# Optimization experiments

Measured on AMD Instinct MI355X. Metric: run time of the kernel, lower is better.

The kernel has to match this reference:

```python
import jax, jax.numpy as jnp
import numpy as np

DIM = 128
HEADS = 4
WIN = (2, 7, 7)
N = WIN[0] * WIN[1] * WIN[2]  # 98
NW = 64
B_ = 2048  # batch(32) * nW(64)
SCALE = (DIM // HEADS) ** -0.5


def _relative_position_index():
    d, h, w = WIN
    coords = np.stack(np.meshgrid(np.arange(d), np.arange(h), np.arange(w), indexing='ij'))
    cf = coords.reshape(3, -1)
    rel = (cf[:, :, None] - cf[:, None, :]).transpose(1, 2, 0)
    rel[:, :, 0] += d - 1
    rel[:, :, 1] += h - 1
    rel[:, :, 2] += w - 1
    rel[:, :, 0] *= (2 * h - 1) * (2 * w - 1)
    rel[:, :, 1] *= 2 * w - 1
    return rel.sum(-1).astype(np.int32)  # [N, N]


def setup_inputs() -> dict:
    key = jax.random.key(0)
    ks = jax.random.split(key, 8)
    table_rows = (2 * WIN[0] - 1) * (2 * WIN[1] - 1) * (2 * WIN[2] - 1)  # 507
    return {
        "x": jax.random.normal(ks[0], (B_, N, DIM), jnp.float32),
        "mask": jax.random.normal(ks[1], (NW, N, N), jnp.float32),
        "qkv_w": jax.random.normal(ks[2], (DIM, 3 * DIM), jnp.float32) * 0.02,
        "qkv_b": jnp.zeros((3 * DIM,), jnp.float32),
        "rel_bias_table": jax.random.normal(ks[3], (table_rows, HEADS), jnp.float32) * 0.02,
        "rel_index": jnp.asarray(_relative_position_index()),
        "proj_w": jax.random.normal(ks[4], (DIM, DIM), jnp.float32) * 0.02,
        "proj_b": jnp.zeros((DIM,), jnp.float32),
    }


def reference(x, mask, qkv_w, qkv_b, rel_bias_table, rel_index, proj_w, proj_b):
    B, n, C = x.shape
    H = HEADS
    hd = C // H
    qkv = x @ qkv_w + qkv_b                              # [B, N, 3C]
    qkv = qkv.reshape(B, n, 3, H, hd).transpose(2, 0, 3, 1, 4)  # [3, B, H, N, hd]
    q, k, v = qkv[0] * SCALE, qkv[1], qkv[2]
    attn = jnp.einsum('bhnd,bhmd->bhnm', q, k)           # [B, H, N, N]
    bias = rel_bias_table[rel_index.reshape(-1)].reshape(n, n, H).transpose(2, 0, 1)
    attn = attn + bias[None]
    nW = mask.shape[0]
    attn = attn.reshape(B // nW, nW, H, n, n) + mask[None, :, None]
    attn = attn.reshape(B, H, n, n)
    attn = jax.nn.softmax(attn, axis=-1)
    out = jnp.einsum('bhnm,bhmd->bnhd', attn, v).reshape(B, n, C)
    return out @ proj_w + proj_b
```

## Files before the change

### kernel.cpp

```cpp
#include <hip/hip_runtime.h>
#include <hip/hip_bf16.h>

typedef __bf16 bf16;
typedef __attribute__((ext_vector_type(8))) __bf16 bf16x8;
typedef __attribute__((ext_vector_type(4))) __bf16 bf16x4;
typedef __attribute__((ext_vector_type(2))) __bf16 bf16x2;
typedef __attribute__((ext_vector_type(4))) float f32x4;

#define NTOK 98
#define NP   112
#define DIM  128
#define NH   4
#define HD   32
#define LOG2E 1.4426950408889634f
#define SCALE_Q2 (0.17677669529663687f * 1.4426950408889634f)
#define SCALE_Q 0.17677669529663687f

#define SXP 136
#define SKP 40
#define SVP 136
#define SPP 136
#define SQP 40
#define STGP 40
#define HREG 2560

#define WS_WTQ   0ULL
#define WS_PT    98304ULL
#define WS_BM    131072ULL
#define WS_BIAS  12976128ULL
#define WS_NEED  13176832ULL

#define PREPA_SCALAR (384*128 + 128*128)
#define PREPA_BIAS   (4*112*28)
#define PREPB_TOTAL  (64*4*112*28)

__global__ __launch_bounds__(256) void prep_a_kernel(
    const float* __restrict__ qkv_w, const float* __restrict__ proj_w,
    const float* __restrict__ table, const int* __restrict__ rel,
    bf16* __restrict__ WTq, bf16* __restrict__ PT2, float* __restrict__ biasT)
{
  int i = blockIdx.x * 256 + threadIdx.x;
  if (i < 384*128) {
    int n = i >> 7, k = i & 127;
    WTq[i] = (bf16)qkv_w[k*384 + n];
  } else if (i < PREPA_SCALAR) {
    int j = i - 384*128; int n = j >> 7, kp = j & 127;
    int blk = kp >> 5, jl = kp & 31;
    int dl = (jl >> 1) + 16*(jl & 1);
    PT2[j] = (bf16)proj_w[(blk*32 + dl)*128 + n];
  } else {
    int g = i - PREPA_SCALAR;
    if (g >= PREPA_BIAS) return;
    int k4 = (g % 28) * 4;
    int rest = g / 28;
    int q = rest % 112;
    int h = rest / 112;
    f32x4 v;
#pragma unroll
    for (int j = 0; j < 4; ++j) {
      int k = k4 + j;
      if (q >= NTOK)      v[j] = 0.f;
      else if (k >= NTOK) v[j] = -1.0e30f;
      else                v[j] = table[rel[q*98 + k]*4 + h] * LOG2E;
    }
    *(f32x4*)(biasT + (h*NP + q)*NP + k4) = v;
  }
}

__global__ __launch_bounds__(256) void prep_b_kernel(
    const float* __restrict__ mask, const float* __restrict__ biasT,
    float* __restrict__ bmt)
{
  int g = blockIdx.x * 256 + threadIdx.x;
  if (g >= PREPB_TOTAL) return;
  int k4 = (g % 28) * 4;
  int rest = g / 28;
  int q = rest % 112;
  int rest2 = rest / 112;
  int h = rest2 & 3;
  int w = rest2 >> 2;
  f32x4 v = *(const f32x4*)(biasT + (h*NP + q)*NP + k4);
  if (q < NTOK) {
    const float* mrow = mask + w*9604 + q*98;
#pragma unroll
    for (int j = 0; j < 4; ++j) {
      int k = k4 + j;
      if (k < NTOK) v[j] = fmaf(mrow[k], LOG2E, v[j]);
    }
  }
  *(f32x4*)(bmt + ((size_t)(w*4 + h))*(NP*NP) + q*NP + k4) = v;
}

__global__ __launch_bounds__(256, 3) void fused_kernel(
    const float* __restrict__ x, const float* __restrict__ qkv_b,
    const float* __restrict__ proj_b,
    const bf16* __restrict__ WTq, const bf16* __restrict__ PT2,
    const float* __restrict__ bmt, float* __restrict__ out)
{
  __shared__ alignas(16) bf16 sA[NP*SXP];
  __shared__ alignas(16) bf16 sB[4*HREG];

  const int b = blockIdx.x, w = b & 63;
  const int tid = threadIdx.x;
  const int wave = tid >> 6, lane = tid & 63;
  const int quad = lane >> 4, l16 = lane & 15;
  const int h = wave;
  const f32x4 fzero = {0.f, 0.f, 0.f, 0.f};

  {
    const float* xb = x + (size_t)b * (NTOK*DIM);
    for (int i = tid; i < NTOK*32; i += 256) {
      int row = i >> 5, c4 = (i & 31) << 2;
      const float4 v = *(const float4*)(xb + row*DIM + c4);
      bf16x4 pk; pk[0]=(bf16)v.x; pk[1]=(bf16)v.y; pk[2]=(bf16)v.z; pk[3]=(bf16)v.w;
      *(bf16x4*)&sA[row*SXP + c4] = pk;
    }
    for (int i = tid; i < 14*32; i += 256) {
      int row = NTOK + (i >> 5), c4 = (i & 31) << 2;
      uint2 z; z.x = 0; z.y = 0;
      *(uint2*)&sA[row*SXP + c4] = z;
    }
  }
  __syncthreads();

  bf16* stg = sB + h*HREG;
  bf16x8 bk[7], aq[7], bv[2][4];

  {
    const int baseK = DIM + h*HD, baseQ = h*HD;
    bf16x8 wK0[4], wK1[4], wQ0[4], wQ1[4];
#pragma unroll
    for (int ks = 0; ks < 4; ++ks) {
      wK0[ks] = *(const bf16x8*)(WTq + (baseK + l16)*DIM + ks*32 + quad*8);
      wK1[ks] = *(const bf16x8*)(WTq + (baseK + 16 + l16)*DIM + ks*32 + quad*8);
      wQ0[ks] = *(const bf16x8*)(WTq + (baseQ + l16)*DIM + ks*32 + quad*8);
      wQ1[ks] = *(const bf16x8*)(WTq + (baseQ + 16 + l16)*DIM + ks*32 + quad*8);
    }
    const float cK0 = qkv_b[baseK + l16], cK1 = qkv_b[baseK + 16 + l16];
    const float cQ0 = qkv_b[baseQ + l16], cQ1 = qkv_b[baseQ + 16 + l16];
#pragma unroll
    for (int mt = 0; mt < 7; ++mt) {
      f32x4 k0 = fzero, k1 = fzero, q0 = fzero, q1 = fzero;
#pragma unroll
      for (int ks = 0; ks < 4; ++ks) {
        const bf16x8 a = *(const bf16x8*)&sA[(mt*16 + l16)*SXP + ks*32 + quad*8];
        k0 = __builtin_amdgcn_mfma_f32_16x16x32_bf16(a, wK0[ks], k0, 0, 0, 0);
        k1 = __builtin_amdgcn_mfma_f32_16x16x32_bf16(a, wK1[ks], k1, 0, 0, 0);
        q0 = __builtin_amdgcn_mfma_f32_16x16x32_bf16(a, wQ0[ks], q0, 0, 0, 0);
        q1 = __builtin_amdgcn_mfma_f32_16x16x32_bf16(a, wQ1[ks], q1, 0, 0, 0);
      }
#pragma unroll
      for (int r = 0; r < 4; ++r) {
        bf16x2 pk; pk[0] = (bf16)(k0[r] + cK0); pk[1] = (bf16)(k1[r] + cK1);
        *(bf16x2*)&stg[(quad*4 + r)*STGP + l16*2] = pk;
        bf16x2 pq; pq[0] = (bf16)((q0[r] + cQ0) * SCALE_Q2);
        pq[1] = (bf16)((q1[r] + cQ1) * SCALE_Q2);
        *(bf16x2*)&stg[(16 + quad*4 + r)*STGP + l16*2] = pq;
      }
      bk[mt] = *(const bf16x8*)&stg[l16*STGP + quad*8];
      aq[mt] = *(const bf16x8*)&stg[(16 + l16)*STGP + quad*8];
    }
  }

  {
    const int baseV = 2*DIM + h*HD;
    bf16x8 wV0[4], wV1[4];
#pragma unroll
    for (int ks = 0; ks < 4; ++ks) {
      wV0[ks] = *(const bf16x8*)(WTq + (baseV + l16)*DIM + ks*32 + quad*8);
      wV1[ks] = *(const bf16x8*)(WTq + (baseV + 16 + l16)*DIM + ks*32 + quad*8);
    }
    const float cV0 = qkv_b[baseV + l16], cV1 = qkv_b[baseV + 16 + l16];
#pragma unroll
    for (int ck = 0; ck < 4; ++ck) {
      bf16* vb = stg + (ck & 1)*1280;
#pragma unroll
      for (int hf = 0; hf < 2; ++hf) {
        const int mt = ck*2 + hf;
        if (mt < 7) {
          f32x4 a0 = fzero, a1 = fzero;
#pragma unroll
          for (int ks = 0; ks < 4; ++ks) {
            const bf16x8 a = *(const bf16x8*)&sA[(mt*16 + l16)*SXP + ks*32 + quad*8];
            a0 = __builtin_amdgcn_mfma_f32_16x16x32_bf16(a, wV0[ks], a0, 0, 0, 0);
            a1 = __builtin_amdgcn_mfma_f32_16x16x32_bf16(a, wV1[ks], a1, 0, 0, 0);
          }
          bf16x4 p0, p1;
#pragma unroll
          for (int r = 0; r < 4; ++r) { p0[r] = (bf16)(a0[r] + cV0); p1[r] = (bf16)(a1[r] + cV1); }
          *(bf16x4*)&vb[l16*STGP + hf*16 + quad*4] = p0;
          *(bf16x4*)&vb[(16 + l16)*STGP + hf*16 + quad*4] = p1;
        } else {
          uint2 z; z.x = 0; z.y = 0;
          *(uint2*)&vb[l16*STGP + hf*16 + quad*4] = z;
          *(uint2*)&vb[(16 + l16)*STGP + hf*16 + quad*4] = z;
        }
      }
      bv[0][ck] = *(const bf16x8*)&vb[l16*STGP + quad*8];
      bv[1][ck] = *(const bf16x8*)&vb[(16 + l16)*STGP + quad*8];
    }
  }
  __syncthreads();

  bf16* sP = stg;
  {
    int row = lane >> 2, c0 = 112 + ((lane & 3) << 2);
    uint2 z; z.x = 0; z.y = 0;
    *(uint2*)&sP[row*SPP + c0] = z;
  }
  const float* bmh = bmt + ((size_t)(w*4 + h))*(NP*NP);

#pragma unroll
  for (int mt = 0; mt < 7; ++mt) {
    const float* bq = bmh + (mt*16 + l16)*NP;
    f32x4 s[7];
#pragma unroll
    for (int nt = 0; nt < 7; ++nt) {
      const f32x4 bm4 = *(const f32x4*)(bq + nt*16 + quad*4);
      s[nt] = __builtin_amdgcn_mfma_f32_16x16x32_bf16(bk[nt], aq[mt], bm4, 0, 0, 0);
    }
#pragma unroll
    for (int nt = 0; nt < 7; ++nt)
#pragma unroll
      for (int r = 0; r < 4; ++r)
        s[nt][r] = __builtin_amdgcn_exp2f(s[nt][r]);
#pragma unroll
    for (int nt = 0; nt < 7; ++nt) {
      bf16x4 pk;
#pragma unroll
      for (int r = 0; r < 4; ++r) pk[r] = (bf16)s[nt][r];
      *(bf16x4*)&sP[l16*SPP + nt*16 + quad*4] = pk;
    }
    f32x4 o0 = fzero, o1 = fzero;
#pragma unroll
    for (int ks = 0; ks < 4; ++ks) {
      const bf16x8 ap = *(const bf16x8*)&sP[l16*SPP + ks*32 + quad*8];
      o0 = __builtin_amdgcn_mfma_f32_16x16x32_bf16(ap, bv[0][ks], o0, 0, 0, 0);
      o1 = __builtin_amdgcn_mfma_f32_16x16x32_bf16(ap, bv[1][ks], o1, 0, 0, 0);
    }
    float rs[7];
#pragma unroll
    for (int nt = 0; nt < 7; ++nt)
      rs[nt] = (s[nt][0] + s[nt][1]) + (s[nt][2] + s[nt][3]);
    float sum = ((rs[0] + rs[1]) + (rs[2] + rs[3])) + ((rs[4] + rs[5]) + rs[6]);
    sum += __shfl_xor(sum, 16);
    sum += __shfl_xor(sum, 32);
    const float inv = __builtin_amdgcn_rcpf(sum);
    float invr[4];
#pragma unroll
    for (int r = 0; r < 4; ++r)
      invr[r] = __shfl(inv, quad*4 + r, 64);
#pragma unroll
    for (int r = 0; r < 4; ++r) {
      bf16x2 ow; ow[0] = (bf16)(o0[r]*invr[r]); ow[1] = (bf16)(o1[r]*invr[r]);
      *(bf16x2*)&sA[(mt*16 + quad*4 + r)*SXP + h*HD + l16*2] = ow;
    }
  }
  __syncthreads();

  float* outb = out + (size_t)b * (NTOK*DIM);
#pragma unroll
  for (int nn = 0; nn < 2; ++nn) {
    const int nt2 = wave + nn*4;
    bf16x8 pf[4];
#pragma unroll
    for (int ks = 0; ks < 4; ++ks)
      pf[ks] = *(const bf16x8*)(PT2 + (nt2*16 + l16)*DIM + ks*32 + quad*8);
    const float pb = proj_b[nt2*16 + l16];
#pragma unroll
    for (int mt = 0; mt < 7; ++mt) {
      f32x4 acc = fzero;
#pragma unroll
      for (int ks = 0; ks < 4; ++ks) {
        const bf16x8 a = *(const bf16x8*)&sA[(mt*16 + l16)*SXP + ks*32 + quad*8];
        acc = __builtin_amdgcn_mfma_f32_16x16x32_bf16(a, pf[ks], acc, 0, 0, 0);
      }
#pragma unroll
      for (int r = 0; r < 4; ++r) {
        const int row = mt*16 + quad*4 + r;
        if (row < NTOK)
          outb[row*DIM + nt2*16 + l16] = acc[r] + pb;
      }
    }
  }
}


__global__ __launch_bounds__(256) void prep_kernel(
    const float* __restrict__ qkv_w, const float* __restrict__ proj_w,
    const float* __restrict__ table, const int* __restrict__ rel_index,
    bf16* __restrict__ WTq, bf16* __restrict__ PT, float* __restrict__ biasf)
{
  int i = blockIdx.x * 256 + threadIdx.x;
  if (i < 384*128) {
    int n = i >> 7, k = i & 127;
    WTq[i] = (bf16)qkv_w[k*384 + n];
  } else if (i < 384*128 + 128*128) {
    int j = i - 384*128; int n = j >> 7, k = j & 127;
    PT[j] = (bf16)proj_w[k*128 + n];
  } else if (i < 384*128 + 128*128 + 98*98) {
    int j = i - (384*128 + 128*128);
    int idx = rel_index[j];
#pragma unroll
    for (int h = 0; h < 4; ++h) biasf[h*9604 + j] = table[idx*4 + h];
  }
}

__global__ __launch_bounds__(512, 2) void win_attn_kernel(
    const float* __restrict__ x, const float* __restrict__ mask,
    const float* __restrict__ qkv_b, const float* __restrict__ proj_b,
    const bf16* __restrict__ WTq, const bf16* __restrict__ PT,
    const float* __restrict__ biasf, float* __restrict__ out)
{
  __shared__ bf16 sX[NP*SXP];
  __shared__ bf16 sK[NH*NP*SKP];
  __shared__ bf16 sVT[NH*HD*SVP];
  __shared__ bf16 sQs[8*16*SQP];
  __shared__ bf16 sPs[8*16*SPP];

  const int b = blockIdx.x;
  const int w = b & 63;
  const int tid = threadIdx.x;
  const int wave = tid >> 6, lane = tid & 63;
  const int quad = lane >> 4, l16 = lane & 15;
  const f32x4 fzero = {0.f, 0.f, 0.f, 0.f};

  {
    const float* xb = x + (size_t)b * (NTOK*DIM);
    for (int i = tid; i < NTOK*32; i += 512) {
      int row = i >> 5, c4 = (i & 31) << 2;
      const float4 v = *(const float4*)(xb + row*DIM + c4);
      bf16x4 pk; pk[0]=(bf16)v.x; pk[1]=(bf16)v.y; pk[2]=(bf16)v.z; pk[3]=(bf16)v.w;
      *(bf16x4*)&sX[row*SXP + c4] = pk;
    }
    for (int i = tid; i < 14*32; i += 512) {
      int row = NTOK + (i >> 5), c4 = (i & 31) << 2;
      uint2 z; z.x = 0; z.y = 0;
      *(uint2*)&sX[row*SXP + c4] = z;
    }
    {
      int h = tid >> 7, rem = tid & 127, d = rem >> 2, c0 = 112 + ((rem & 3) << 2);
      uint2 z; z.x = 0; z.y = 0;
      *(uint2*)&sVT[(h*HD + d)*SVP + c0] = z;
    }
  }
  __syncthreads();

#pragma unroll
  for (int j = 0; j < 2; ++j) {
    const int job = wave*2 + j;
    const int h = job >> 2, part = job & 3;
    const bool isK = part < 2;
    const int ncol = (isK ? DIM + h*HD + part*16 : 2*DIM + h*HD + (part-2)*16) + l16;
    bf16x8 bfr[4];
#pragma unroll
    for (int ks = 0; ks < 4; ++ks)
      bfr[ks] = *(const bf16x8*)(WTq + ncol*DIM + ks*32 + quad*8);
    const float cb = qkv_b[ncol];
#pragma unroll
    for (int mt = 0; mt < 7; ++mt) {
      f32x4 acc = fzero;
#pragma unroll
      for (int ks = 0; ks < 4; ++ks) {
        const bf16x8 a = *(const bf16x8*)&sX[(mt*16 + l16)*SXP + ks*32 + quad*8];
        acc = __builtin_amdgcn_mfma_f32_16x16x32_bf16(a, bfr[ks], acc, 0, 0, 0);
      }
      const int tb = mt*16 + quad*4;
      if (isK) {
        const int d = part*16 + l16;
#pragma unroll
        for (int r = 0; r < 4; ++r)
          sK[(h*NP + tb + r)*SKP + d] = (bf16)(acc[r] + cb);
      } else {
        const int d = (part-2)*16 + l16;
        bf16x4 pk;
#pragma unroll
        for (int r = 0; r < 4; ++r) pk[r] = (bf16)(acc[r] + cb);
        *(bf16x4*)&sVT[(h*HD + d)*SVP + tb] = pk;
      }
    }
  }
  __syncthreads();

  {
    const int h = wave >> 1, sub = wave & 1;
    bf16x8 qb[2][4];
#pragma unroll
    for (int nt2 = 0; nt2 < 2; ++nt2)
#pragma unroll
      for (int ks = 0; ks < 4; ++ks)
        qb[nt2][ks] = *(const bf16x8*)(WTq + (h*HD + nt2*16 + l16)*DIM + ks*32 + quad*8);
    const float qbias0 = qkv_b[h*HD + l16];
    const float qbias1 = qkv_b[h*HD + 16 + l16];
    bf16* sQ = sQs + wave*16*SQP;
    bf16* sP = sPs + wave*16*SPP;
    {
      int row = lane >> 2, c0 = 112 + ((lane & 3) << 2);
      uint2 z; z.x = 0; z.y = 0;
      *(uint2*)&sP[row*SPP + c0] = z;
    }
    const float* bias_h = biasf + h*9604;
    const float* mask_w = mask + w*9604;

    f32x4 oacc0 = fzero, oacc1 = fzero;
#pragma unroll 1
    for (int it = 0; it < 4; ++it) {
      const int mt = sub + it*2;
      const bool valid = mt < 7;
      if (valid) {
        f32x4 qa0 = fzero, qa1 = fzero;
#pragma unroll
        for (int ks = 0; ks < 4; ++ks) {
          const bf16x8 a = *(const bf16x8*)&sX[(mt*16 + l16)*SXP + ks*32 + quad*8];
          qa0 = __builtin_amdgcn_mfma_f32_16x16x32_bf16(a, qb[0][ks], qa0, 0, 0, 0);
          qa1 = __builtin_amdgcn_mfma_f32_16x16x32_bf16(a, qb[1][ks], qa1, 0, 0, 0);
        }
#pragma unroll
        for (int r = 0; r < 4; ++r) {
          sQ[(quad*4 + r)*SQP + l16]      = (bf16)((qa0[r] + qbias0) * SCALE_Q);
          sQ[(quad*4 + r)*SQP + 16 + l16] = (bf16)((qa1[r] + qbias1) * SCALE_Q);
        }
        const bf16x8 aq = *(const bf16x8*)&sQ[l16*SQP + quad*8];
        f32x4 s[7];
#pragma unroll
        for (int nt = 0; nt < 7; ++nt) {
          const bf16x8 bk2 = *(const bf16x8*)&sK[(h*NP + nt*16 + l16)*SKP + quad*8];
          s[nt] = __builtin_amdgcn_mfma_f32_16x16x32_bf16(aq, bk2, fzero, 0, 0, 0);
        }
#pragma unroll
        for (int r = 0; r < 4; ++r) {
          const int row = mt*16 + quad*4 + r;
          const bool rowok = row < NTOK;
          float mx = -3.0e38f;
#pragma unroll
          for (int nt = 0; nt < 7; ++nt) {
            const int col = nt*16 + l16;
            float sv;
            if (rowok && col < NTOK)
              sv = s[nt][r] + bias_h[row*NTOK + col] + mask_w[row*NTOK + col];
            else
              sv = -1.0e30f;
            s[nt][r] = sv;
            mx = fmaxf(mx, sv);
          }
#pragma unroll
          for (int off = 1; off < 16; off <<= 1)
            mx = fmaxf(mx, __shfl_xor(mx, off, 64));
          float sum = 0.f;
#pragma unroll
          for (int nt = 0; nt < 7; ++nt) {
            const float p = __expf(s[nt][r] - mx);
            s[nt][r] = p;
            sum += p;
          }
#pragma unroll
          for (int off = 1; off < 16; off <<= 1)
            sum += __shfl_xor(sum, off, 64);
          const float inv = __builtin_amdgcn_rcpf(sum);
#pragma unroll
          for (int nt = 0; nt < 7; ++nt)
            sP[(quad*4 + r)*SPP + nt*16 + l16] = (bf16)(s[nt][r] * inv);
        }
        oacc0 = fzero; oacc1 = fzero;
#pragma unroll
        for (int ks = 0; ks < 4; ++ks) {
          const bf16x8 ap = *(const bf16x8*)&sP[l16*SPP + ks*32 + quad*8];
          const bf16x8 bv0 = *(const bf16x8*)&sVT[(h*HD + l16)*SVP + ks*32 + quad*8];
          const bf16x8 bv1 = *(const bf16x8*)&sVT[(h*HD + 16 + l16)*SVP + ks*32 + quad*8];
          oacc0 = __builtin_amdgcn_mfma_f32_16x16x32_bf16(ap, bv0, oacc0, 0, 0, 0);
          oacc1 = __builtin_amdgcn_mfma_f32_16x16x32_bf16(ap, bv1, oacc1, 0, 0, 0);
        }
      }
      __syncthreads();
      if (valid) {
#pragma unroll
        for (int r = 0; r < 4; ++r) {
          sX[(mt*16 + quad*4 + r)*SXP + h*HD + l16]      = (bf16)(oacc0[r]);
          sX[(mt*16 + quad*4 + r)*SXP + h*HD + 16 + l16] = (bf16)(oacc1[r]);
        }
      }
    }
  }
  __syncthreads();

  {
    const int nt = wave;
    bf16x8 pbf[4];
#pragma unroll
    for (int ks = 0; ks < 4; ++ks)
      pbf[ks] = *(const bf16x8*)(PT + (nt*16 + l16)*DIM + ks*32 + quad*8);
    const float pb = proj_b[nt*16 + l16];
    float* outb = out + (size_t)b * (NTOK*DIM);
#pragma unroll
    for (int mt = 0; mt < 7; ++mt) {
      f32x4 acc = fzero;
#pragma unroll
      for (int ks = 0; ks < 4; ++ks) {
        const bf16x8 a = *(const bf16x8*)&sX[(mt*16 + l16)*SXP + ks*32 + quad*8];
        acc = __builtin_amdgcn_mfma_f32_16x16x32_bf16(a, pbf[ks], acc, 0, 0, 0);
      }
#pragma unroll
      for (int r = 0; r < 4; ++r) {
        const int row = mt*16 + quad*4 + r;
        if (row < NTOK)
          outb[row*DIM + nt*16 + l16] = acc[r] + pb;
      }
    }
  }
}

extern "C" void kernel_launch(void* const* d_in, const int* in_sizes, int n_in,
                              void* d_out, int out_size, void* d_ws, size_t ws_size,
                              hipStream_t stream)
{
  const float* x      = (const float*)d_in[0];
  const float* mask   = (const float*)d_in[1];
  const float* qkv_w  = (const float*)d_in[2];
  const float* qkv_b  = (const float*)d_in[3];
  const float* table  = (const float*)d_in[4];
  const int*   rel    = (const int*)d_in[5];
  const float* proj_w = (const float*)d_in[6];
  const float* proj_b = (const float*)d_in[7];
  float* out = (float*)d_out;
  char* ws = (char*)d_ws;

  if (ws_size >= WS_NEED) {
    bf16*  WTq   = (bf16*)(ws + WS_WTQ);
    bf16*  PT2   = (bf16*)(ws + WS_PT);
    float* bmt   = (float*)(ws + WS_BM);
    float* biasT = (float*)(ws + WS_BIAS);

    const int prepa_total = PREPA_SCALAR + PREPA_BIAS;
    prep_a_kernel<<<(prepa_total + 255)/256, 256, 0, stream>>>(
        qkv_w, proj_w, table, rel, WTq, PT2, biasT);
    prep_b_kernel<<<(PREPB_TOTAL + 255)/256, 256, 0, stream>>>(mask, biasT, bmt);
    fused_kernel<<<2048, 256, 0, stream>>>(x, qkv_b, proj_b, WTq, PT2, bmt, out);
  } else {
    bf16*  WTq   = (bf16*)(ws + WS_WTQ);
    bf16*  PT    = (bf16*)(ws + WS_PT);
    float* biasf = (float*)(ws + WS_BM);
    const int prep_total = 384*128 + 128*128 + 98*98;
    prep_kernel<<<(prep_total + 255)/256, 256, 0, stream>>>(qkv_w, proj_w, table, rel, WTq, PT, biasf);
    win_attn_kernel<<<2048, 512, 0, stream>>>(x, mask, qkv_b, proj_b, WTq, PT, biasf, out);
  }
}
```

Baseline: 267.7 us.

## Store bias+mask table in fp16 and group blocks by window for cache reuse

The precomputed bias+mask table is now stored in half precision, which halves its size and the traffic of reading it in the fused kernel. The padding sentinel becomes -28000 so it still fits in fp16. Block indices are remapped so that consecutive blocks share the same mask window, which is meant to improve L2 reuse of that window's bias slab. The cost is fp16 rounding of the logits bias, a small accuracy risk.

```diff
diff --git a/kernel.cpp b/kernel.cpp
--- a/kernel.cpp
+++ b/kernel.cpp
@@ -6,6 +6,8 @@
 typedef __attribute__((ext_vector_type(4))) __bf16 bf16x4;
 typedef __attribute__((ext_vector_type(2))) __bf16 bf16x2;
 typedef __attribute__((ext_vector_type(4))) float f32x4;
+typedef __attribute__((ext_vector_type(8))) _Float16 f16x8;
+typedef __attribute__((ext_vector_type(4))) _Float16 f16x4;
 
 #define NTOK 98
 #define NP   112
@@ -15,6 +17,7 @@
 #define LOG2E 1.4426950408889634f
 #define SCALE_Q2 (0.17677669529663687f * 1.4426950408889634f)
 #define SCALE_Q 0.17677669529663687f
+#define KSENT  (-28000.0f)
 
 #define SXP 136
 #define SKP 40
@@ -27,12 +30,12 @@
 #define WS_WTQ   0ULL
 #define WS_PT    98304ULL
 #define WS_BM    131072ULL
-#define WS_BIAS  12976128ULL
-#define WS_NEED  13176832ULL
+#define WS_BIAS  6553600ULL
+#define WS_NEED  6754304ULL
 
 #define PREPA_SCALAR (384*128 + 128*128)
 #define PREPA_BIAS   (4*112*28)
-#define PREPB_TOTAL  (64*4*112*28)
+#define PREPB_TOTAL  (64*4*112*14)
 
 __global__ __launch_bounds__(256) void prep_a_kernel(
     const float* __restrict__ qkv_w, const float* __restrict__ proj_w,
@@ -60,7 +63,7 @@
     for (int j = 0; j < 4; ++j) {
       int k = k4 + j;
       if (q >= NTOK)      v[j] = 0.f;
-      else if (k >= NTOK) v[j] = -1.0e30f;
+      else if (k >= NTOK) v[j] = KSENT;
       else                v[j] = table[rel[q*98 + k]*4 + h] * LOG2E;
     }
     *(f32x4*)(biasT + (h*NP + q)*NP + k4) = v;
@@ -69,38 +72,46 @@
 
 __global__ __launch_bounds__(256) void prep_b_kernel(
     const float* __restrict__ mask, const float* __restrict__ biasT,
-    float* __restrict__ bmt)
+    _Float16* __restrict__ bmt)
 {
   int g = blockIdx.x * 256 + threadIdx.x;
   if (g >= PREPB_TOTAL) return;
-  int k4 = (g % 28) * 4;
-  int rest = g / 28;
+  int k8 = (g % 14) * 8;
+  int rest = g / 14;
   int q = rest % 112;
   int rest2 = rest / 112;
   int h = rest2 & 3;
   int w = rest2 >> 2;
-  f32x4 v = *(const f32x4*)(biasT + (h*NP + q)*NP + k4);
+  const float* bt = biasT + (h*NP + q)*NP + k8;
+  f16x8 o;
   if (q < NTOK) {
     const float* mrow = mask + w*9604 + q*98;
 #pragma unroll
-    for (int j = 0; j < 4; ++j) {
-      int k = k4 + j;
-      if (k < NTOK) v[j] = fmaf(mrow[k], LOG2E, v[j]);
-    }
-  }
-  *(f32x4*)(bmt + ((size_t)(w*4 + h))*(NP*NP) + q*NP + k4) = v;
+    for (int j = 0; j < 8; ++j) {
+      int k = k8 + j;
+      float v = bt[j];
+      if (k < NTOK) v = fmaf(mrow[k], LOG2E, v);
+      o[j] = (_Float16)v;
+    }
+  } else {
+#pragma unroll
+    for (int j = 0; j < 8; ++j) o[j] = (_Float16)bt[j];
+  }
+  *(f16x8*)(bmt + ((size_t)(w*4 + h))*(NP*NP) + q*NP + k8) = o;
 }
 
 __global__ __launch_bounds__(256, 3) void fused_kernel(
     const float* __restrict__ x, const float* __restrict__ qkv_b,
     const float* __restrict__ proj_b,
     const bf16* __restrict__ WTq, const bf16* __restrict__ PT2,
-    const float* __restrict__ bmt, float* __restrict__ out)
+    const _Float16* __restrict__ bmt, float* __restrict__ out)
 {
   __shared__ alignas(16) bf16 sA[NP*SXP];
   __shared__ alignas(16) bf16 sB[4*HREG];
 
-  const int b = blockIdx.x, w = b & 63;
+  const int b = blockIdx.x;
+  const int win = ((b & 31) << 6) | (b >> 5);
+  const int w = b >> 5;
   const int tid = threadIdx.x;
   const int wave = tid >> 6, lane = tid & 63;
   const int quad = lane >> 4, l16 = lane & 15;
@@ -108,7 +119,7 @@
   const f32x4 fzero = {0.f, 0.f, 0.f, 0.f};
 
   {
-    const float* xb = x + (size_t)b * (NTOK*DIM);
+    const float* xb = x + (size_t)win * (NTOK*DIM);
     for (int i = tid; i < NTOK*32; i += 256) {
       int row = i >> 5, c4 = (i & 31) << 2;
       const float4 v = *(const float4*)(xb + row*DIM + c4);
@@ -208,15 +219,18 @@
     uint2 z; z.x = 0; z.y = 0;
     *(uint2*)&sP[row*SPP + c0] = z;
   }
-  const float* bmh = bmt + ((size_t)(w*4 + h))*(NP*NP);
+  const _Float16* bmh = bmt + ((size_t)(w*4 + h))*(NP*NP);
 
 #pragma unroll
   for (int mt = 0; mt < 7; ++mt) {
-    const float* bq = bmh + (mt*16 + l16)*NP;
+    const _Float16* bq = bmh + (mt*16 + l16)*NP;
     f32x4 s[7];
 #pragma unroll
     for (int nt = 0; nt < 7; ++nt) {
-      const f32x4 bm4 = *(const f32x4*)(bq + nt*16 + quad*4);
+      const f16x4 bh = *(const f16x4*)(bq + nt*16 + quad*4);
+      f32x4 bm4;
+#pragma unroll
+      for (int r = 0; r < 4; ++r) bm4[r] = (float)bh[r];
       s[nt] = __builtin_amdgcn_mfma_f32_16x16x32_bf16(bk[nt], aq[mt], bm4, 0, 0, 0);
     }
 #pragma unroll
@@ -258,7 +272,7 @@
   }
   __syncthreads();
 
-  float* outb = out + (size_t)b * (NTOK*DIM);
+  float* outb = out + (size_t)win * (NTOK*DIM);
 #pragma unroll
   for (int nn = 0; nn < 2; ++nn) {
     const int nt2 = wave + nn*4;
@@ -525,10 +539,10 @@
   char* ws = (char*)d_ws;
 
   if (ws_size >= WS_NEED) {
-    bf16*  WTq   = (bf16*)(ws + WS_WTQ);
-    bf16*  PT2   = (bf16*)(ws + WS_PT);
-    float* bmt   = (float*)(ws + WS_BM);
-    float* biasT = (float*)(ws + WS_BIAS);
+    bf16*     WTq   = (bf16*)(ws + WS_WTQ);
+    bf16*     PT2   = (bf16*)(ws + WS_PT);
+    _Float16* bmt   = (_Float16*)(ws + WS_BM);
+    float*    biasT = (float*)(ws + WS_BIAS);
 
     const int prepa_total = PREPA_SCALAR + PREPA_BIAS;
     prep_a_kernel<<<(prepa_total + 255)/256, 256, 0, stream>>>(
```

Measured after the change: 273.3 us. 1.02x slower.
